# Optimization experiments

Measured on AMD Instinct MI355X. Metric: run time of the kernel, lower is better.

The kernel has to match this reference:

```python
import jax, jax.numpy as jnp
import numpy as np

B, V, H, W = 1, 88, 128, 256
P = 2                  # patch size
D = 128                # hidden_dim = embed_dim // latent_ratio = 1536 // 12
NG = 12                # n_group (== latent_ratio)
NH = 2                 # heads per attention = num_heads // latent_ratio = 24 // 12
E = NG * D             # embed_dim = 1536
HD = D // NH
SCALE = HD ** -0.5

# Static ragged group index sets derived from the variable names (sizes 7,7,7,7,7,9,9,9,9,9,17,6).
# Pressure-level vars are ordered z,q,t,u,v per level; levels [50..400]=7 levels, [50..600]=9 levels.
_off = {'z': 0, 'q': 1, 't': 2, 'u': 3, 'v': 4}
GROUPS = []
for name in ['u1', 'v1', 't1', 'q1', 'z1', 'u2', 'v2', 't2', 'q2', 'z2', 'surf', 'const']:
    if name[-1] in '12':
        nl = 7 if name[-1] == '1' else 9
        GROUPS.append(np.array([5 * li + _off[name[0]] for li in range(nl)]))
    elif name == 'surf':
        GROUPS.append(np.arange(65, 82))   # 17 surface vars
    else:
        GROUPS.append(np.arange(82, 88))   # 6 constant vars


def setup_inputs() -> dict:
    key = jax.random.key(0)
    ks = jax.random.split(key, 16)
    return {
        "x": jax.random.normal(ks[0], (B, V, H, W), jnp.float32),
        # per-variable conv patch-embed weights, flattened to (V, P*P, D)
        "conv_w": jax.random.normal(ks[1], (V, P * P, D), jnp.float32) * 0.05,
        "conv_b": jax.random.normal(ks[2], (V, D), jnp.float32) * 0.02,
        "channel_embed": jax.random.normal(ks[3], (1, V, D), jnp.float32) * 0.02,
        "channel_query": jax.random.uniform(ks[4], (1, NG, D), jnp.float32) * 0.2,
        # 12 distinct MultiheadAttention modules: packed in_proj (3D, D) + out_proj
        "grp_in_w": jax.random.normal(ks[5], (NG, 3 * D, D), jnp.float32) * 0.05,
        "grp_in_b": jax.random.normal(ks[6], (NG, 3 * D), jnp.float32) * 0.02,
        "grp_out_w": jax.random.normal(ks[7], (NG, D, D), jnp.float32) * 0.05,
        "grp_out_b": jax.random.normal(ks[8], (NG, D), jnp.float32) * 0.02,
        "ens_query": jax.random.uniform(ks[9], (1, NG, D), jnp.float32) * 0.2,
        "ens_in_w": jax.random.normal(ks[10], (3 * D, D), jnp.float32) * 0.05,
        "ens_in_b": jax.random.normal(ks[11], (3 * D,), jnp.float32) * 0.02,
        "ens_out_w": jax.random.normal(ks[12], (D, D), jnp.float32) * 0.05,
        "ens_out_b": jax.random.normal(ks[13], (D,), jnp.float32) * 0.02,
        "ln_gamma": jnp.ones((E,), jnp.float32),
        "ln_beta": jnp.zeros((E,), jnp.float32),
    }


def reference(x, conv_w, conv_b, channel_embed, channel_query,
              grp_in_w, grp_in_b, grp_out_w, grp_out_b,
              ens_query, ens_in_w, ens_in_b, ens_out_w, ens_out_b,
              ln_gamma, ln_beta):
    b, v, h, w = x.shape
    hp, wp = h // P, w // P
    L = hp * wp
    # non-overlapping stride-P conv with 1 input channel == patchify + per-variable matmul
    patches = x.reshape(b, v, hp, P, wp, P).transpose(0, 1, 2, 4, 3, 5).reshape(b, v, L, P * P)
    xe = jnp.einsum('bvlp,vpd->bvld', patches, conv_w) + conv_b[None, :, None, :]
    xe = xe + channel_embed[:, :, None, :]                 # (B, V, L, D)
    xn = xe.transpose(0, 2, 1, 3).reshape(b * L, v, D)     # (N, V, D), N = B*L

    outs = []
    for i, ids in enumerate(GROUPS):                       # 12 fixed, structurally distinct groups
        kv = xn[:, ids, :]                                 # (N, g, D), ragged g
        Wq, Wk, Wv = grp_in_w[i, :D], grp_in_w[i, D:2 * D], grp_in_w[i, 2 * D:]
        bq, bk, bv = grp_in_b[i, :D], grp_in_b[i, D:2 * D], grp_in_b[i, 2 * D:]
        q = (channel_query[0, i] @ Wq.T + bq).reshape(NH, HD)
        k = (kv @ Wk.T + bk).reshape(-1, len(ids), NH, HD)
        vv = (kv @ Wv.T + bv).reshape(-1, len(ids), NH, HD)
        a = jax.nn.softmax(jnp.einsum('hd,nghd->nhg', q, k) * SCALE, axis=-1)
        o = jnp.einsum('nhg,nghd->nhd', a, vv).reshape(-1, D)
        outs.append(o @ grp_out_w[i].T + grp_out_b[i])
    out = jnp.stack(outs, axis=1)                          # (N, 12, D)

    Wq, Wk, Wv = ens_in_w[:D], ens_in_w[D:2 * D], ens_in_w[2 * D:]
    bq, bk, bv = ens_in_b[:D], ens_in_b[D:2 * D], ens_in_b[2 * D:]
    q = (ens_query[0] @ Wq.T + bq).reshape(NG, NH, HD)     # 12 ensemble query tokens
    k = (out @ Wk.T + bk).reshape(-1, NG, NH, HD)
    vv = (out @ Wv.T + bv).reshape(-1, NG, NH, HD)
    a = jax.nn.softmax(jnp.einsum('thd,nshd->nhts', q, k) * SCALE, axis=-1)
    r = jnp.einsum('nhts,nshd->nthd', a, vv).reshape(-1, NG, D)
    r = (r @ ens_out_w.T + ens_out_b).reshape(b, L, E)     # (B, L, embed_dim)

    mu = r.mean(axis=-1, keepdims=True)
    var = r.var(axis=-1, keepdims=True)
    return (r - mu) * jax.lax.rsqrt(var + 1e-5) * ln_gamma + ln_beta
```

## Files before the change

kernel.cpp:

```cpp
#include <hip/hip_runtime.h>


typedef __attribute__((ext_vector_type(8))) short short8;
typedef __attribute__((ext_vector_type(4))) float f32x4;

__constant__ int GOFF[13] = {0,7,14,21,28,35,44,53,62,71,80,97,103};
__constant__ int K5A[12]  = {35,35,35,35,35,45,45,45,45,45,85,30};
__constant__ int SLOTS3[12] = {3,3,3,3,3,3,3,3,3,3,6,2};
__constant__ int FOFFA[12] = {0,3,6,9,12,15,18,21,24,27,30,36};
__constant__ int GSLOT[103] = {
  3,8,13,18,23,28,33,
  4,9,14,19,24,29,34,
  2,7,12,17,22,27,32,
  1,6,11,16,21,26,31,
  0,5,10,15,20,25,30,
  3,8,13,18,23,28,33,38,43,
  4,9,14,19,24,29,34,39,44,
  2,7,12,17,22,27,32,37,42,
  1,6,11,16,21,26,31,36,41,
  0,5,10,15,20,25,30,35,40,
  45,46,47,48,49,50,51,52,53,54,55,56,57,58,59,60,61,
  62,63,64,65,66,67};
__constant__ int GIDX[103] = {
  0,0,0,0,0,0,0, 1,1,1,1,1,1,1, 2,2,2,2,2,2,2, 3,3,3,3,3,3,3, 4,4,4,4,4,4,4,
  5,5,5,5,5,5,5,5,5, 6,6,6,6,6,6,6,6,6, 7,7,7,7,7,7,7,7,7, 8,8,8,8,8,8,8,8,8,
  9,9,9,9,9,9,9,9,9,
  10,10,10,10,10,10,10,10,10,10,10,10,10,10,10,10,10,
  11,11,11,11,11,11};
__constant__ int TGI[38] = {0,0,0,1,1,1,2,2,2,3,3,3,4,4,4,5,5,5,6,6,6,7,7,7,
                            8,8,8,9,9,9,10,10,10,10,10,10,11,11};
__constant__ int TNT[38] = {0,1,2,0,1,2,0,1,2,0,1,2,0,1,2,0,1,2,0,1,2,0,1,2,
                            0,1,2,0,1,2,0,1,2,3,4,5,0,1};

constexpr int cSLOTS[12] = {3,3,3,3,3,3,3,3,3,3,6,2};
constexpr int cFOFFA[12] = {0,3,6,9,12,15,18,21,24,27,30,36};

#define QK_GRP 0
#define QK_ENS 3072
#define QB_GRP 6144
#define QB_ENS 6176
#define CGRP   6208
#define CENS   7744
#define CWQ_BYTE   43776
#define MPL_BYTE   50432
#define CW2_BYTE   836864
#define MEB_BYTE   1623296
#define QKEB_BYTE  1688832
#define FWS_BYTE   1697024

__device__ __forceinline__ float bf2f(unsigned short s) {
  return __uint_as_float(((unsigned)s) << 16);
}
__device__ __forceinline__ unsigned short f2bf(float f) {
  unsigned u = __float_as_uint(f);
  u += 0x7fffu + ((u >> 16) & 1u);
  return (unsigned short)(u >> 16);
}

__global__ void hwe_p1(const float* __restrict__ giw, const float* __restrict__ gib,
                       const float* __restrict__ gow, const float* __restrict__ gob,
                       const float* __restrict__ cq,  const float* __restrict__ eq,
                       const float* __restrict__ eiw, const float* __restrict__ eib,
                       const float* __restrict__ eow, const float* __restrict__ eob,
                       const float* __restrict__ cw,  const float* __restrict__ cb,
                       const float* __restrict__ ce,
                       float* __restrict__ wsf, unsigned short* __restrict__ MA,
                       unsigned short* __restrict__ CW2,
                       unsigned short* __restrict__ MeB, unsigned short* __restrict__ Fws) {
  int blk = blockIdx.x, tid = threadIdx.x;
  int wave = tid >> 6, lane = tid & 63;
  if (blk < 48) {
    __shared__ float qf[64];
    bool ens = blk >= 24;
    int bi = ens ? blk - 24 : blk;
    int i = bi >> 1, h = bi & 1;
    const float* W  = ens ? eiw : giw + i*49152;
    const float* bv = ens ? eib : gib + i*384;
    const float* qv = ens ? eq + i*128 : cq + i*128;
    for (int it = 0; it < 16; ++it) {
      int dp = it*4 + wave;
      const float* wrow = W + (h*64 + dp)*128;
      float acc = wrow[lane]*qv[lane] + wrow[lane+64]*qv[lane+64];
#pragma unroll
      for (int off = 32; off > 0; off >>= 1) acc += __shfl_down(acc, off);
      if (lane == 0) qf[dp] = acc + bv[h*64 + dp];
    }
    __syncthreads();
    if (tid < 128) {
      int e = tid;
      const float* Wk = W + (128 + h*64)*128 + e;
      float a0=0.f,a1=0.f,a2=0.f,a3=0.f;
      for (int dp = 0; dp < 64; dp += 4) {
        a0 += qf[dp+0] * Wk[(dp+0)*128];
        a1 += qf[dp+1] * Wk[(dp+1)*128];
        a2 += qf[dp+2] * Wk[(dp+2)*128];
        a3 += qf[dp+3] * Wk[(dp+3)*128];
      }
      wsf[(ens ? QK_ENS : QK_GRP) + bi*128 + e] = (a0+a1)+(a2+a3);
    }
    if (wave == 3) {
      float acc = qf[lane] * bv[128 + h*64 + lane];
#pragma unroll
      for (int off = 32; off > 0; off >>= 1) acc += __shfl_down(acc, off);
      if (lane == 0) wsf[(ens ? QB_ENS : QB_GRP) + bi] = acc;
    }
  } else if (blk < 1584) {
    int b2 = blk - 48;
    int gi = b2 >> 7, r = b2 & 127;
    int ep = tid, h = ep >> 7, e = ep & 127;
    const float* wo = gow + gi*16384 + r*128 + h*64;
    const float* wv = giw + gi*49152 + (256 + h*64)*128 + e;
    float a0=0.f,a1=0.f,a2=0.f,a3=0.f;
    for (int hd = 0; hd < 64; hd += 4) {
      a0 += wo[hd+0] * wv[(hd+0)*128];
      a1 += wo[hd+1] * wv[(hd+1)*128];
      a2 += wo[hd+2] * wv[(hd+2)*128];
      a3 += wo[hd+3] * wv[(hd+3)*128];
    }
    float acc = (a0+a1)+(a2+a3);
    int mt = r >> 4, lr = r & 15, kt = e >> 5, q = (e >> 3) & 3, j = e & 7;
    MA[(((gi*2 + h)*8 + mt)*4 + kt)*512 + (q*16 + lr)*8 + j] = f2bf(acc);
  } else if (blk < 1712) {
    int f2 = (blk - 1584)*256 + tid;
    int r = f2 >> 8, ep = f2 & 255;
    int h = ep >> 7, e = ep & 127;
    const float* wo = eow + r*128 + h*64;
    const float* wv = eiw + (256 + h*64)*128 + e;
    float a0=0.f,a1=0.f,a2=0.f,a3=0.f;
    for (int hd = 0; hd < 64; hd += 4) {
      a0 += wo[hd+0] * wv[(hd+0)*128];
      a1 += wo[hd+1] * wv[(hd+1)*128];
      a2 += wo[hd+2] * wv[(hd+2)*128];
      a3 += wo[hd+3] * wv[(hd+3)*128];
    }
    float acc = (a0+a1)+(a2+a3);
    int mt = r >> 4, lr = r & 15, kt = ep >> 5, q = (ep >> 3) & 3, j = ep & 7;
    MeB[((mt*8 + kt)*64 + (q*16 + lr))*8 + j] = f2bf(acc);
  } else if (blk < 2096) {
    int id = (blk - 1712)*4 + wave;
    int i = id >> 7, d = id & 127;
    const float* wrow = gow + i*16384 + d*128;
    const float* bvv = gib + i*384 + 256;
    float acc = wrow[lane]*bvv[lane] + wrow[lane+64]*bvv[lane+64];
#pragma unroll
    for (int off = 32; off > 0; off >>= 1) acc += __shfl_down(acc, off);
    if (lane == 0) wsf[CGRP + id] = acc + gob[i*128 + d];
  } else if (blk < 2128) {
    int d = (blk - 2096)*4 + wave;
    const float* wrow = eow + d*128;
    const float* bvv = eib + 256;
    float acc = wrow[lane]*bvv[lane] + wrow[lane+64]*bvv[lane+64];
#pragma unroll
    for (int off = 32; off > 0; off >>= 1) acc += __shfl_down(acc, off);
    if (lane == 0) wsf[CENS + d] = acc + eob[d];
  } else if (blk < 2166) {
    int tile = blk - 2128;
    int gi = TGI[tile], nt = TNT[tile];
    int kt = tid >> 6;
    int l15b = tid & 15, quadb = (tid >> 4) & 3;
    int k = nt*16 + l15b;
    int e = kt*32 + quadb*8;
    unsigned short vv[8];
    if (k < K5A[gi]) {
      int q = (k*205) >> 10;
      int pp = k - q*5;
      int s = GSLOT[GOFF[gi] + q];
      int v = (s < 45) ? s : s + 20;
      if (pp < 4) {
        const float* src = cw + (v*4 + pp)*128 + e;
#pragma unroll
        for (int j = 0; j < 8; ++j) vv[j] = f2bf(src[j]);
      } else {
        const float* b1 = cb + v*128 + e;
        const float* c1 = ce + v*128 + e;
#pragma unroll
        for (int j = 0; j < 8; ++j) vv[j] = f2bf(b1[j] + c1[j]);
      }
    } else {
#pragma unroll
      for (int j = 0; j < 8; ++j) vv[j] = 0;
    }
    unsigned short* dst = CW2 + (tile*4 + kt)*512 + (tid & 63)*8;
#pragma unroll
    for (int j = 0; j < 8; ++j) dst[j] = vv[j];
  } else {
    int idx = (blk - 2166)*256 + tid;
    if (idx < 19456) ((uint4*)Fws)[idx] = (uint4){0,0,0,0};
  }
}

__global__ void hwe_p2(const float* __restrict__ cw, const float* __restrict__ cb,
                       const float* __restrict__ ce,
                       const unsigned short* __restrict__ MA,
                       const unsigned short* __restrict__ CW2,
                       const float* __restrict__ wsf,
                       unsigned short* __restrict__ Fws,
                       unsigned short* __restrict__ qkeB, float* __restrict__ cwq) {
  int blk = blockIdx.x, tid = threadIdx.x;
  int wave = tid >> 6, lane = tid & 63;
  int quad = lane >> 4, l15 = lane & 15;
  if (blk < 192) {
    int gi = blk >> 4, h = (blk >> 3) & 1, mt = blk & 7;
    int K5 = K5A[gi], S = SLOTS3[gi];
    const unsigned short* MAp = MA + (((gi*2 + h)*8 + mt)*4)*512 + lane*8;
    short8 a[4];
#pragma unroll
    for (int kt = 0; kt < 4; ++kt)
      a[kt] = *(const short8*)(MAp + kt*512);
    for (int nt = wave; nt < S; nt += 4) {
      const unsigned short* Bp = CW2 + (FOFFA[gi] + nt)*2048 + lane*8;
      f32x4 acc = {0.f,0.f,0.f,0.f};
#pragma unroll
      for (int kt = 0; kt < 4; ++kt) {
        short8 b = *(const short8*)(Bp + kt*512);
        acc = __builtin_amdgcn_mfma_f32_16x16x32_bf16(a[kt], b, acc, 0, 0, 0);
      }
      int k = nt*16 + l15;
      if (k < K5) {
        int kpp = h*K5 + k;
        int base = (FOFFA[gi]*8 + mt*S + (kpp >> 5))*512
                 + ((kpp >> 3) & 3)*128 + (kpp & 7);
#pragma unroll
        for (int reg = 0; reg < 4; ++reg) {
          int rr = quad*4 + reg;
          Fws[base + rr*8] = f2bf(acc[reg]);
        }
      }
    }
  } else if (blk < 208) {
    int f4 = (blk - 192)*256 + tid;
    int ln = (f4 >> 3) & 63, j = f4 & 7;
    int th = ((f4 >> 11) & 1)*16 + (ln & 15);
    int kt = (f4 >> 9) & 3;
    float val = (th < 24) ? wsf[QK_ENS + th*128 + kt*32 + (ln >> 4)*8 + j] : 0.f;
    qkeB[f4] = f2bf(val);
  } else {
    int wid = (blk - 208)*4 + wave;
    if (wid < 206) {
      int gg = wid >> 1, h = wid & 1;
      int gi = GIDX[gg];
      int s = GSLOT[gg];
      int v = (s < 45) ? s : s + 20;
      const float* qk = wsf + QK_GRP + (gi*2 + h)*128;
      float q0 = qk[lane], q1 = qk[lane + 64];
      float a[5];
#pragma unroll
      for (int pp = 0; pp < 4; ++pp)
        a[pp] = cw[(v*4 + pp)*128 + lane]*q0 + cw[(v*4 + pp)*128 + lane + 64]*q1;
      a[4] = (cb[v*128 + lane] + ce[v*128 + lane])*q0 +
             (cb[v*128 + lane + 64] + ce[v*128 + lane + 64])*q1;
#pragma unroll
      for (int off = 32; off > 0; off >>= 1)
#pragma unroll
        for (int kk = 0; kk < 5; ++kk) a[kk] += __shfl_down(a[kk], off);
      if (lane == 0) {
        float* o = cwq + (gg*2 + h)*8;
        o[0] = a[0]*0.125f; o[1] = a[1]*0.125f; o[2] = a[2]*0.125f; o[3] = a[3]*0.125f;
        o[4] = (a[4] + wsf[QB_GRP + gi*2 + h]) * 0.125f;
      }
    }
  }
}

__global__ __launch_bounds__(256, 3) void hwe_main(
    const float* __restrict__ x,
    const float* __restrict__ lgam, const float* __restrict__ lbet,
    const float* __restrict__ wsf,  const float* __restrict__ cwq,
    const unsigned short* __restrict__ Fws, const unsigned short* __restrict__ MeB,
    const unsigned short* __restrict__ qkeB,
    float* __restrict__ out) {
  __shared__ __align__(16) unsigned char smem[53632];
  unsigned short* xpB   = (unsigned short*)(smem);
  unsigned short* scb   = (unsigned short*)(smem + 4352);
  unsigned short* wpAll = (unsigned short*)(smem + 7680);
  unsigned short* Gl    = (unsigned short*)(smem);
  unsigned short* apB   = (unsigned short*)(smem + 20480);
  unsigned short* sce2  = (unsigned short*)(smem);
  unsigned short* outg2 = (unsigned short*)(smem + 28672);
  float*          stats = (float*)(smem + 53504);

  const int tid  = threadIdx.x;
  const int wave = tid >> 6;
  const int lane = tid & 63;
  const int quad = lane >> 4;
  const int l15  = lane & 15;

  const int hi   = blockIdx.x >> 4;
  const int wib  = (blockIdx.x & 15) << 3;
  const int nbase = hi*128 + wib;

  for (int idx = tid; idx < 1088; idx += 256) {
    int c2 = idx & 7, r = (idx >> 3) & 1, s = idx >> 4;
    int v = (s < 45) ? s : s + 20;
    const float2 xv = *(const float2*)(x + (v*128 + 2*hi + r)*256 + 2*wib + c2*2);
    unsigned pk = (unsigned)f2bf(xv.x) | ((unsigned)f2bf(xv.y) << 16);
    *(unsigned*)(xpB + (c2*68 + s)*4 + r*2) = pk;
  }
  if (tid < 64) ((unsigned*)outg2)[96*64 + tid] = 0u;
  __syncthreads();

  for (int idx = tid; idx < 1648; idx += 256) {
    int h = idx & 1, p = (idx >> 1) & 7, gg = idx >> 4;
    int s = GSLOT[gg];
    const float* c = cwq + (gg*2 + h)*8;
    const unsigned short* xr = xpB + (p*68 + s)*4;
    float acc = c[4] + bf2f(xr[0])*c[0] + bf2f(xr[1])*c[1]
                     + bf2f(xr[2])*c[2] + bf2f(xr[3])*c[3];
    scb[(p*2 + h)*104 + gg] = f2bf(acc);
  }
  __syncthreads();

  if (tid < 192) {
    int gi = tid % 12, h = (tid / 12) & 1, p = tid / 24;
    int go = GOFF[gi], G = GOFF[gi+1] - go;
    unsigned short* row = scb + (p*2 + h)*104 + go;
    float ev[17];
    float m = -1e30f;
#pragma unroll
    for (int g = 0; g < 17; ++g) {
      ev[g] = (g < G) ? bf2f(row[g]) : -1e30f;
      m = fmaxf(m, ev[g]);
    }
    float ssum = 0.f;
#pragma unroll
    for (int g = 0; g < 17; ++g) {
      float e = __expf(ev[g] - m);
      ev[g] = e;
      if (g < G) ssum += e;
    }
    float inv = 1.f / ssum;
#pragma unroll
    for (int g = 0; g < 17; ++g)
      if (g < G) row[g] = f2bf(ev[g] * inv);
  }
  __syncthreads();

#pragma unroll
  for (int hb = 0; hb < 2; ++hb) {
    const int nsl = hb ? 20 : 18;
    const int sbase = hb ? 18 : 0;

    short8 fA[6], fB[6];
    float4 cgA, cgB;
    auto fws_issue = [&](int I, short8 (&buf)[6], float4& cg) {
      int gi = hb*6 + (I >> 1);
      int S  = cSLOTS[gi];
      int mt = (I & 1)*4 + wave;
      const unsigned short* fp = Fws + (cFOFFA[gi]*8 + mt*S)*512 + lane*8;
#pragma unroll
      for (int kt = 0; kt < 6; ++kt)
        if (kt < S) buf[kt] = *(const short8*)(fp + kt*512);
      cg = *(const float4*)(wsf + CGRP + gi*128 + mt*16 + quad*4);
    };
    auto fws_compute = [&](int I, short8 (&buf)[6], const float4& cg) {
      int gi = hb*6 + (I >> 1);
      int S  = cSLOTS[gi];
      int mt = (I & 1)*4 + wave;
      int lbase = cFOFFA[gi] - sbase;
      f32x4 acc = {0.f,0.f,0.f,0.f};
#pragma unroll
      for (int kt = 0; kt < 6; ++kt)
        if (kt < S) {
          short8 b = *(const short8*)(wpAll + (lbase + kt)*512 + lane*8);
          acc = __builtin_amdgcn_mfma_f32_16x16x32_bf16(buf[kt], b, acc, 0, 0, 0);
        }
      if (l15 < 8) {
        int p = l15;
        int rb = mt*16 + quad*4;
        unsigned short t0 = f2bf(acc[0] + cg.x);
        unsigned short t1 = f2bf(acc[1] + cg.y);
        unsigned short t2 = f2bf(acc[2] + cg.z);
        unsigned short t3 = f2bf(acc[3] + cg.w);
        uint2 w;
        w.x = (unsigned)t0 | ((unsigned)t1 << 16);
        w.y = (unsigned)t2 | ((unsigned)t3 << 16);
        int row = gi*8 + p;
        int ch = (rb >> 3) ^ ((gi ^ p) & 7);
        *(uint2*)(outg2 + row*128 + ch*8 + (rb & 7)) = w;
      }
    };

    fws_issue(0, fA, cgA);

    {
      const int nposs = nsl * 512;
      for (int pos = tid*4; pos < nposs; pos += 1024) {
        int pf = (pos >> 3) & 15;
        uint2 w2 = {0u, 0u};
        if (pf < 8) {
          int ls = pos >> 9;
          int qd = (pos >> 7) & 3;
          int j0 = pos & 7;
          int p  = pf;
          int gil, K5, fo, goffB, c0, stp;
          if (hb == 0) {
            gil = (ls>=3)+(ls>=6)+(ls>=9)+(ls>=12)+(ls>=15);
            K5 = (gil < 5) ? 35 : 45;
            fo = gil*3;
            goffB = gil*7;
            c0 = (gil==0)?3:(gil==1)?4:(gil==2)?2:(gil==3)?1:(gil==4)?0:3;
            stp = 5;
          } else {
            gil = (ls>=3)+(ls>=6)+(ls>=9)+(ls>=12)+(ls>=18);
            K5 = (gil < 4) ? 45 : (gil == 4) ? 85 : 30;
            fo = (gil < 5) ? gil*3 : 18;
            goffB = (gil < 5) ? (44 + gil*9) : 97;
            c0 = (gil==0)?4:(gil==1)?2:(gil==2)?1:(gil==3)?0:(gil==4)?45:62;
            stp = (gil < 4) ? 5 : 1;
          }
          int kbase = (ls - fo)*32 + qd*8 + j0;
          unsigned short vv[4];
#pragma unroll
          for (int jj = 0; jj < 4; ++jj) {
            int kpp = kbase + jj;
            int h = (kpp >= K5) ? 1 : 0;
            int k = kpp - (h ? K5 : 0);
            int q = (k*205) >> 10;
            int pp = k - q*5;
            int gg = goffB + q;
            int s = c0 + q*stp;
            float a  = bf2f(scb[(p*2 + h)*104 + gg]);
            float xv = bf2f(xpB[(p*68 + s)*4 + pp]);
            float val = (pp < 4) ? a * xv : a;
            if (kpp >= 2*K5) val = 0.f;
            vv[jj] = f2bf(val);
          }
          w2.x = (unsigned)vv[0] | ((unsigned)vv[1] << 16);
          w2.y = (unsigned)vv[2] | ((unsigned)vv[3] << 16);
        }
        *(uint2*)(wpAll + pos) = w2;
      }
    }
    __syncthreads();

#pragma unroll
    for (int ii = 0; ii < 6; ++ii) {
      fws_issue(ii*2 + 1, fB, cgB);
      fws_compute(ii*2, fA, cgA);
      if (ii < 5) fws_issue(ii*2 + 2, fA, cgA);
      fws_compute(ii*2 + 1, fB, cgB);
    }
    __syncthreads();
  }

#pragma unroll
  for (int ti = 0; ti < 3; ++ti) {
    int T = wave*3 + ti;
    int mtp = T >> 1, ntp = T & 1;
    int rowA = mtp*16 + l15;
    int sx = ((rowA >> 3) ^ rowA) & 7;
    f32x4 acc = {0.f,0.f,0.f,0.f};
#pragma unroll
    for (int kt = 0; kt < 4; ++kt) {
      short8 a = *(const short8*)(outg2 + rowA*128 + (((kt*4 + quad) ^ sx) << 3));
      short8 b = *(const short8*)(qkeB + ((ntp*4 + kt)*64 + lane)*8);
      acc = __builtin_amdgcn_mfma_f32_16x16x32_bf16(a, b, acc, 0, 0, 0);
    }
    int th = ntp*16 + l15;
    if (th < 24) {
      float qb = wsf[QB_ENS + th];
#pragma unroll
      for (int reg = 0; reg < 4; ++reg) {
        int rowE = mtp*16 + quad*4 + reg;
        sce2[((rowE & 7)*24 + th)*16 + (rowE >> 3)] = f2bf((acc[reg] + qb) * 0.125f);
      }
    }
  }
  __syncthreads();

  if (tid < 192) {
    unsigned short* row = sce2 + tid*16;
    float ev[12];
    float m = -1e30f;
#pragma unroll
    for (int s = 0; s < 12; ++s) { ev[s] = bf2f(row[s]); m = fmaxf(m, ev[s]); }
    float ssum = 0.f;
#pragma unroll
    for (int s = 0; s < 12; ++s) { float e = __expf(ev[s] - m); ev[s] = e; ssum += e; }
    float inv = 1.f / ssum;
#pragma unroll
    for (int s = 0; s < 12; ++s) row[s] = f2bf(ev[s] * inv);
  }
  __syncthreads();

  for (int idx = tid; idx < 4096; idx += 256) {
    int p = idx >> 9, r9 = idx & 511;
    int ln = r9 >> 3, j = r9 & 7;
    int t = ln & 15, qd = ln >> 4;
    int kpp = qd*8 + j;
    int h = kpp >> 4, s = kpp & 15;
    unsigned short v = 0;
    if (s < 12 && t < 12) v = sce2[(p*24 + t*2 + h)*16 + s];
    apB[p*512 + ln*8 + j] = v;
  }
  float cens0[4], cens1[4];
  {
    float4 c0 = *(const float4*)(wsf + CENS + (wave*2 + 0)*16 + quad*4);
    float4 c1 = *(const float4*)(wsf + CENS + (wave*2 + 1)*16 + quad*4);
    cens0[0]=c0.x; cens0[1]=c0.y; cens0[2]=c0.z; cens0[3]=c0.w;
    cens1[0]=c1.x; cens1[1]=c1.y; cens1[2]=c1.z; cens1[3]=c1.w;
  }
  short8 meAr[16];
#pragma unroll
  for (int mi = 0; mi < 2; ++mi)
#pragma unroll
    for (int h = 0; h < 2; ++h)
#pragma unroll
      for (int kt = 0; kt < 4; ++kt)
        meAr[(mi*2 + h)*4 + kt] =
          *(const short8*)(MeB + (((wave*2 + mi)*8 + h*4 + kt)*64 + lane)*8);
  __syncthreads();

  for (int pp2 = 0; pp2 < 4; ++pp2) {
    f32x4 g[2][2][2];
#pragma unroll
    for (int lp = 0; lp < 2; ++lp)
#pragma unroll
      for (int mi = 0; mi < 2; ++mi)
#pragma unroll
        for (int h = 0; h < 2; ++h) g[lp][mi][h] = (f32x4){0.f,0.f,0.f,0.f};
#pragma unroll
    for (int lp = 0; lp < 2; ++lp) {
      int p = pp2*2 + lp;
      int brow = (l15 < 12) ? (l15*8 + p) : 96;
      int sx = ((brow >> 3) ^ brow) & 7;
#pragma unroll
      for (int h = 0; h < 2; ++h) {
#pragma unroll
        for (int kt = 0; kt < 4; ++kt) {
          short8 b = *(const short8*)(outg2 + brow*128 + (((kt*4 + quad) ^ sx) << 3));
          g[lp][0][h] = __builtin_amdgcn_mfma_f32_16x16x32_bf16(
              meAr[(0*2 + h)*4 + kt], b, g[lp][0][h], 0, 0, 0);
          g[lp][1][h] = __builtin_amdgcn_mfma_f32_16x16x32_bf16(
              meAr[(1*2 + h)*4 + kt], b, g[lp][1][h], 0, 0, 0);
        }
      }
    }
#pragma unroll
    for (int lp = 0; lp < 2; ++lp)
#pragma unroll
      for (int mi = 0; mi < 2; ++mi)
#pragma unroll
        for (int h = 0; h < 2; ++h)
#pragma unroll
          for (int reg = 0; reg < 4; ++reg) {
            int r = (wave*2 + mi)*16 + quad*4 + reg;
            Gl[lp*5120 + r*40 + h*16 + l15] = f2bf(g[lp][mi][h][reg]);
          }

    f32x4 rr[2][2];
    float s1[2] = {0.f, 0.f}, s2[2] = {0.f, 0.f};
#pragma unroll
    for (int lp = 0; lp < 2; ++lp) {
      int p = pp2*2 + lp;
      short8 bfrag = *(const short8*)(apB + p*512 + lane*8);
#pragma unroll
      for (int mi = 0; mi < 2; ++mi) {
        int mt2 = wave*2 + mi;
        short8 afrag = *(const short8*)(Gl + lp*5120 + (mt2*16 + l15)*40 + quad*8);
        f32x4 acc = {0.f,0.f,0.f,0.f};
        acc = __builtin_amdgcn_mfma_f32_16x16x32_bf16(afrag, bfrag, acc, 0, 0, 0);
#pragma unroll
        for (int reg = 0; reg < 4; ++reg)
          acc[reg] += (mi ? cens1[reg] : cens0[reg]);
        rr[lp][mi] = acc;
        if (l15 < 12) {
#pragma unroll
          for (int reg = 0; reg < 4; ++reg) {
            float v = acc[reg];
            s1[lp] += v; s2[lp] += v*v;
          }
        }
      }
    }
#pragma unroll
    for (int off = 32; off > 0; off >>= 1) {
#pragma unroll
      for (int lp = 0; lp < 2; ++lp) {
        s1[lp] += __shfl_xor(s1[lp], off);
        s2[lp] += __shfl_xor(s2[lp], off);
      }
    }
    int sb = (pp2 & 1) << 4;
    if (lane == 0) {
#pragma unroll
      for (int lp = 0; lp < 2; ++lp) {
        stats[sb + lp*4 + wave] = s1[lp];
        stats[sb + 8 + lp*4 + wave] = s2[lp];
      }
    }
    __syncthreads();
#pragma unroll
    for (int lp = 0; lp < 2; ++lp) {
      float t1 = stats[sb+lp*4+0] + stats[sb+lp*4+1] + stats[sb+lp*4+2] + stats[sb+lp*4+3];
      float t2 = stats[sb+8+lp*4+0] + stats[sb+8+lp*4+1] + stats[sb+8+lp*4+2] + stats[sb+8+lp*4+3];
      float mean = t1 * (1.f/1536.f);
      float var  = t2 * (1.f/1536.f) - mean*mean;
      float rstd = rsqrtf(var + 1e-5f);
      if (l15 < 12) {
        long nrow = (long)(nbase + pp2*2 + lp) * 1536;
#pragma unroll
        for (int mi = 0; mi < 2; ++mi) {
          int rb = (wave*2 + mi)*16 + quad*4;
          int j = l15*128 + rb;
          float4 gm = *(const float4*)(lgam + j);
          float4 bt = *(const float4*)(lbet + j);
          float4 o;
          o.x = (rr[lp][mi][0] - mean)*rstd*gm.x + bt.x;
          o.y = (rr[lp][mi][1] - mean)*rstd*gm.y + bt.y;
          o.z = (rr[lp][mi][2] - mean)*rstd*gm.z + bt.z;
          o.w = (rr[lp][mi][3] - mean)*rstd*gm.w + bt.w;
          *(float4*)(out + nrow + j) = o;
        }
      }
    }
  }
}

extern "C" void kernel_launch(void* const* d_in, const int* in_sizes, int n_in,
                              void* d_out, int out_size, void* d_ws, size_t ws_size,
                              hipStream_t stream) {
  const float* x   = (const float*)d_in[0];
  const float* cw  = (const float*)d_in[1];
  const float* cb  = (const float*)d_in[2];
  const float* ce  = (const float*)d_in[3];
  const float* cq  = (const float*)d_in[4];
  const float* giw = (const float*)d_in[5];
  const float* gib = (const float*)d_in[6];
  const float* gow = (const float*)d_in[7];
  const float* gob = (const float*)d_in[8];
  const float* eq  = (const float*)d_in[9];
  const float* eiw = (const float*)d_in[10];
  const float* eib = (const float*)d_in[11];
  const float* eow = (const float*)d_in[12];
  const float* eob = (const float*)d_in[13];
  const float* lg  = (const float*)d_in[14];
  const float* lb  = (const float*)d_in[15];

  float* wsf = (float*)d_ws;
  float* cwq = (float*)((char*)d_ws + CWQ_BYTE);
  unsigned short* MA   = (unsigned short*)((char*)d_ws + MPL_BYTE);
  unsigned short* CW2  = (unsigned short*)((char*)d_ws + CW2_BYTE);
  unsigned short* MeB  = (unsigned short*)((char*)d_ws + MEB_BYTE);
  unsigned short* qkeB = (unsigned short*)((char*)d_ws + QKEB_BYTE);
  unsigned short* Fws  = (unsigned short*)((char*)d_ws + FWS_BYTE);

  hwe_p1<<<2242, 256, 0, stream>>>(giw, gib, gow, gob, cq, eq, eiw, eib, eow, eob,
                                   cw, cb, ce, wsf, MA, CW2, MeB, Fws);
  hwe_p2<<<260, 256, 0, stream>>>(cw, cb, ce, MA, CW2, wsf, Fws, qkeB, cwq);
  hwe_main<<<1024, 256, 0, stream>>>(x, lg, lb, wsf, cwq, Fws, MeB, qkeB,
                                     (float*)d_out);
}
```

Baseline: 177.6 us.

## Shrink LDS footprint to raise occupancy from 3 to 4 blocks per CU

Reduces the kernel's shared memory from about 53.6KB to 40.6KB and raises launch bounds to 4 blocks per CU. To fit, it stages the grouped-attention weighted inputs in six two-group phases instead of two six-group halves, and packs the softmax score buffer more tightly. It also drops the apB staging buffer by building MFMA B fragments directly from the score buffer, and reuses a single Gl tile per position. The cost is more barriers and phases, extra per-lane masking work, and added register pressure under the tighter launch bound.

```diff
diff --git a/kernel.cpp b/kernel.cpp
--- a/kernel.cpp
+++ b/kernel.cpp
@@ -34,6 +34,10 @@
 
 constexpr int cSLOTS[12] = {3,3,3,3,3,3,3,3,3,3,6,2};
 constexpr int cFOFFA[12] = {0,3,6,9,12,15,18,21,24,27,30,36};
+constexpr int cK5[12]    = {35,35,35,35,35,45,45,45,45,45,85,30};
+constexpr int cGOFFC[12] = {0,7,14,21,28,35,44,53,62,71,80,97};
+constexpr int cC0[12]    = {3,4,2,1,0,3,4,2,1,0,45,62};
+constexpr int cSTP[12]   = {5,5,5,5,5,5,5,5,5,5,1,1};
 
 #define QK_GRP 0
 #define QK_ENS 3072
@@ -262,22 +266,21 @@
   }
 }
 
-__global__ __launch_bounds__(256, 3) void hwe_main(
+__global__ __launch_bounds__(256, 4) void hwe_main(
     const float* __restrict__ x,
     const float* __restrict__ lgam, const float* __restrict__ lbet,
     const float* __restrict__ wsf,  const float* __restrict__ cwq,
     const unsigned short* __restrict__ Fws, const unsigned short* __restrict__ MeB,
     const unsigned short* __restrict__ qkeB,
     float* __restrict__ out) {
-  __shared__ __align__(16) unsigned char smem[53632];
+  __shared__ __align__(16) unsigned char smem[40576];
   unsigned short* xpB   = (unsigned short*)(smem);
   unsigned short* scb   = (unsigned short*)(smem + 4352);
   unsigned short* wpAll = (unsigned short*)(smem + 7680);
   unsigned short* Gl    = (unsigned short*)(smem);
-  unsigned short* apB   = (unsigned short*)(smem + 20480);
-  unsigned short* sce2  = (unsigned short*)(smem);
-  unsigned short* outg2 = (unsigned short*)(smem + 28672);
-  float*          stats = (float*)(smem + 53504);
+  unsigned short* sce2  = (unsigned short*)(smem + 10240);
+  unsigned short* outg2 = (unsigned short*)(smem + 15872);
+  float*          stats = (float*)(smem + 40448);
 
   const int tid  = threadIdx.x;
   const int wave = tid >> 6;
@@ -296,7 +299,6 @@
     unsigned pk = (unsigned)f2bf(xv.x) | ((unsigned)f2bf(xv.y) << 16);
     *(unsigned*)(xpB + (c2*68 + s)*4 + r*2) = pk;
   }
-  if (tid < 64) ((unsigned*)outg2)[96*64 + tid] = 0u;
   __syncthreads();
 
   for (int idx = tid; idx < 1648; idx += 256) {
@@ -335,28 +337,22 @@
   }
   __syncthreads();
 
-#pragma unroll
-  for (int hb = 0; hb < 2; ++hb) {
-    const int nsl = hb ? 20 : 18;
-    const int sbase = hb ? 18 : 0;
-
+  {
     short8 fA[6], fB[6];
     float4 cgA, cgB;
-    auto fws_issue = [&](int I, short8 (&buf)[6], float4& cg) {
-      int gi = hb*6 + (I >> 1);
-      int S  = cSLOTS[gi];
-      int mt = (I & 1)*4 + wave;
+    auto fws_issue = [&](int gi, int mh, short8 (&buf)[6], float4& cg) {
+      int S = cSLOTS[gi];
+      int mt = mh*4 + wave;
       const unsigned short* fp = Fws + (cFOFFA[gi]*8 + mt*S)*512 + lane*8;
 #pragma unroll
       for (int kt = 0; kt < 6; ++kt)
         if (kt < S) buf[kt] = *(const short8*)(fp + kt*512);
       cg = *(const float4*)(wsf + CGRP + gi*128 + mt*16 + quad*4);
     };
-    auto fws_compute = [&](int I, short8 (&buf)[6], const float4& cg) {
-      int gi = hb*6 + (I >> 1);
-      int S  = cSLOTS[gi];
-      int mt = (I & 1)*4 + wave;
-      int lbase = cFOFFA[gi] - sbase;
+    auto fws_compute = [&](int gi, int mh, int lbase, short8 (&buf)[6],
+                           const float4& cg) {
+      int S = cSLOTS[gi];
+      int mt = mh*4 + wave;
       f32x4 acc = {0.f,0.f,0.f,0.f};
 #pragma unroll
       for (int kt = 0; kt < 6; ++kt)
@@ -380,68 +376,83 @@
       }
     };
 
-    fws_issue(0, fA, cgA);
-
-    {
-      const int nposs = nsl * 512;
-      for (int pos = tid*4; pos < nposs; pos += 1024) {
-        int pf = (pos >> 3) & 15;
-        uint2 w2 = {0u, 0u};
-        if (pf < 8) {
-          int ls = pos >> 9;
-          int qd = (pos >> 7) & 3;
-          int j0 = pos & 7;
-          int p  = pf;
-          int gil, K5, fo, goffB, c0, stp;
-          if (hb == 0) {
-            gil = (ls>=3)+(ls>=6)+(ls>=9)+(ls>=12)+(ls>=15);
-            K5 = (gil < 5) ? 35 : 45;
-            fo = gil*3;
-            goffB = gil*7;
-            c0 = (gil==0)?3:(gil==1)?4:(gil==2)?2:(gil==3)?1:(gil==4)?0:3;
-            stp = 5;
-          } else {
-            gil = (ls>=3)+(ls>=6)+(ls>=9)+(ls>=12)+(ls>=18);
-            K5 = (gil < 4) ? 45 : (gil == 4) ? 85 : 30;
-            fo = (gil < 5) ? gil*3 : 18;
-            goffB = (gil < 5) ? (44 + gil*9) : 97;
-            c0 = (gil==0)?4:(gil==1)?2:(gil==2)?1:(gil==3)?0:(gil==4)?45:62;
-            stp = (gil < 4) ? 5 : 1;
+    fws_issue(0, 0, fA, cgA);
+
+#pragma unroll
+    for (int ph = 0; ph < 6; ++ph) {
+      const int g0 = 2*ph;
+      const int S0 = cSLOTS[g0];
+      const int nsl = S0 + cSLOTS[g0+1];
+
+      {
+        const int nposs = nsl * 512;
+        for (int pos = tid*4; pos < nposs; pos += 1024) {
+          int pf = (pos >> 3) & 15;
+          uint2 w2 = {0u, 0u};
+          if (pf < 8) {
+            int ls = pos >> 9;
+            int qd = (pos >> 7) & 3;
+            int j0 = pos & 7;
+            int p  = pf;
+            bool gsel = (ls >= S0);
+            int lsl   = gsel ? ls - S0 : ls;
+            int K5    = gsel ? cK5[g0+1]    : cK5[g0];
+            int goffB = gsel ? cGOFFC[g0+1] : cGOFFC[g0];
+            int c0    = gsel ? cC0[g0+1]    : cC0[g0];
+            int stp   = gsel ? cSTP[g0+1]   : cSTP[g0];
+            int kbase = lsl*32 + qd*8 + j0;
+            unsigned short vv[4];
+#pragma unroll
+            for (int jj = 0; jj < 4; ++jj) {
+              int kpp = kbase + jj;
+              int h = (kpp >= K5) ? 1 : 0;
+              int k = kpp - (h ? K5 : 0);
+              int q = (k*205) >> 10;
+              int pp = k - q*5;
+              int gg = goffB + q;
+              int s = c0 + q*stp;
+              float a  = bf2f(scb[(p*2 + h)*104 + gg]);
+              float xv = bf2f(xpB[(p*68 + s)*4 + pp]);
+              float val = (pp < 4) ? a * xv : a;
+              if (kpp >= 2*K5) val = 0.f;
+              vv[jj] = f2bf(val);
+            }
+            w2.x = (unsigned)vv[0] | ((unsigned)vv[1] << 16);
+            w2.y = (unsigned)vv[2] | ((unsigned)vv[3] << 16);
           }
-          int kbase = (ls - fo)*32 + qd*8 + j0;
-          unsigned short vv[4];
-#pragma unroll
-          for (int jj = 0; jj < 4; ++jj) {
-            int kpp = kbase + jj;
-            int h = (kpp >= K5) ? 1 : 0;
-            int k = kpp - (h ? K5 : 0);
-            int q = (k*205) >> 10;
-            int pp = k - q*5;
-            int gg = goffB + q;
-            int s = c0 + q*stp;
-            float a  = bf2f(scb[(p*2 + h)*104 + gg]);
-            float xv = bf2f(xpB[(p*68 + s)*4 + pp]);
-            float val = (pp < 4) ? a * xv : a;
-            if (kpp >= 2*K5) val = 0.f;
-            vv[jj] = f2bf(val);
-          }
-          w2.x = (unsigned)vv[0] | ((unsigned)vv[1] << 16);
-          w2.y = (unsigned)vv[2] | ((unsigned)vv[3] << 16);
+          *(uint2*)(wpAll + pos) = w2;
         }
-        *(uint2*)(wpAll + pos) = w2;
-      }
-    }
-    __syncthreads();
-
-#pragma unroll
-    for (int ii = 0; ii < 6; ++ii) {
-      fws_issue(ii*2 + 1, fB, cgB);
-      fws_compute(ii*2, fA, cgA);
-      if (ii < 5) fws_issue(ii*2 + 2, fA, cgA);
-      fws_compute(ii*2 + 1, fB, cgB);
-    }
-    __syncthreads();
-  }
+      }
+      __syncthreads();
+
+      fws_issue(g0+0, 1, fB, cgB);
+      fws_compute(g0+0, 0, 0,  fA, cgA);
+      fws_issue(g0+1, 0, fA, cgA);
+      fws_compute(g0+0, 1, 0,  fB, cgB);
+      fws_issue(g0+1, 1, fB, cgB);
+      fws_compute(g0+1, 0, S0, fA, cgA);
+      if (ph < 5) fws_issue(g0+2, 0, fA, cgA);
+      fws_compute(g0+1, 1, S0, fB, cgB);
+      __syncthreads();
+    }
+  }
+
+  float cens0[4], cens1[4];
+  {
+    float4 c0 = *(const float4*)(wsf + CENS + (wave*2 + 0)*16 + quad*4);
+    float4 c1 = *(const float4*)(wsf + CENS + (wave*2 + 1)*16 + quad*4);
+    cens0[0]=c0.x; cens0[1]=c0.y; cens0[2]=c0.z; cens0[3]=c0.w;
+    cens1[0]=c1.x; cens1[1]=c1.y; cens1[2]=c1.z; cens1[3]=c1.w;
+  }
+  short8 meAr[16];
+#pragma unroll
+  for (int mi = 0; mi < 2; ++mi)
+#pragma unroll
+    for (int h = 0; h < 2; ++h)
+#pragma unroll
+      for (int kt = 0; kt < 4; ++kt)
+        meAr[(mi*2 + h)*4 + kt] =
+          *(const short8*)(MeB + (((wave*2 + mi)*8 + h*4 + kt)*64 + lane)*8);
 
 #pragma unroll
   for (int ti = 0; ti < 3; ++ti) {
@@ -462,14 +473,14 @@
 #pragma unroll
       for (int reg = 0; reg < 4; ++reg) {
         int rowE = mtp*16 + quad*4 + reg;
-        sce2[((rowE & 7)*24 + th)*16 + (rowE >> 3)] = f2bf((acc[reg] + qb) * 0.125f);
+        sce2[((rowE & 7)*24 + th)*12 + (rowE >> 3)] = f2bf((acc[reg] + qb) * 0.125f);
       }
     }
   }
   __syncthreads();
 
   if (tid < 192) {
-    unsigned short* row = sce2 + tid*16;
+    unsigned short* row = sce2 + tid*12;
     float ev[12];
     float m = -1e30f;
 #pragma unroll
@@ -483,34 +494,6 @@
   }
   __syncthreads();
 
-  for (int idx = tid; idx < 4096; idx += 256) {
-    int p = idx >> 9, r9 = idx & 511;
-    int ln = r9 >> 3, j = r9 & 7;
-    int t = ln & 15, qd = ln >> 4;
-    int kpp = qd*8 + j;
-    int h = kpp >> 4, s = kpp & 15;
-    unsigned short v = 0;
-    if (s < 12 && t < 12) v = sce2[(p*24 + t*2 + h)*16 + s];
-    apB[p*512 + ln*8 + j] = v;
-  }
-  float cens0[4], cens1[4];
-  {
-    float4 c0 = *(const float4*)(wsf + CENS + (wave*2 + 0)*16 + quad*4);
-    float4 c1 = *(const float4*)(wsf + CENS + (wave*2 + 1)*16 + quad*4);
-    cens0[0]=c0.x; cens0[1]=c0.y; cens0[2]=c0.z; cens0[3]=c0.w;
-    cens1[0]=c1.x; cens1[1]=c1.y; cens1[2]=c1.z; cens1[3]=c1.w;
-  }
-  short8 meAr[16];
-#pragma unroll
-  for (int mi = 0; mi < 2; ++mi)
-#pragma unroll
-    for (int h = 0; h < 2; ++h)
-#pragma unroll
-      for (int kt = 0; kt < 4; ++kt)
-        meAr[(mi*2 + h)*4 + kt] =
-          *(const short8*)(MeB + (((wave*2 + mi)*8 + h*4 + kt)*64 + lane)*8);
-  __syncthreads();
-
   for (int pp2 = 0; pp2 < 4; ++pp2) {
     f32x4 g[2][2][2];
 #pragma unroll
@@ -522,13 +505,14 @@
 #pragma unroll
     for (int lp = 0; lp < 2; ++lp) {
       int p = pp2*2 + lp;
-      int brow = (l15 < 12) ? (l15*8 + p) : 96;
+      int brow = (l15 < 12) ? (l15*8 + p) : 0;
       int sx = ((brow >> 3) ^ brow) & 7;
 #pragma unroll
       for (int h = 0; h < 2; ++h) {
 #pragma unroll
         for (int kt = 0; kt < 4; ++kt) {
           short8 b = *(const short8*)(outg2 + brow*128 + (((kt*4 + quad) ^ sx) << 3));
+          if (l15 >= 12) b = (short8){0,0,0,0,0,0,0,0};
           g[lp][0][h] = __builtin_amdgcn_mfma_f32_16x16x32_bf16(
               meAr[(0*2 + h)*4 + kt], b, g[lp][0][h], 0, 0, 0);
           g[lp][1][h] = __builtin_amdgcn_mfma_f32_16x16x32_bf16(
@@ -536,8 +520,12 @@
         }
       }
     }
-#pragma unroll
-    for (int lp = 0; lp < 2; ++lp)
+
+    f32x4 rr[2][2];
+    float s1[2] = {0.f, 0.f}, s2[2] = {0.f, 0.f};
+#pragma unroll
+    for (int lp = 0; lp < 2; ++lp) {
+      int p = pp2*2 + lp;
 #pragma unroll
       for (int mi = 0; mi < 2; ++mi)
 #pragma unroll
@@ -545,21 +533,24 @@
 #pragma unroll
           for (int reg = 0; reg < 4; ++reg) {
             int r = (wave*2 + mi)*16 + quad*4 + reg;
-            Gl[lp*5120 + r*40 + h*16 + l15] = f2bf(g[lp][mi][h][reg]);
+            Gl[r*40 + h*16 + l15] = f2bf(g[lp][mi][h][reg]);
           }
-
-    f32x4 rr[2][2];
-    float s1[2] = {0.f, 0.f}, s2[2] = {0.f, 0.f};
-#pragma unroll
-    for (int lp = 0; lp < 2; ++lp) {
-      int p = pp2*2 + lp;
-      short8 bfrag = *(const short8*)(apB + p*512 + lane*8);
+      short8 af0 = *(const short8*)(Gl + ((wave*2 + 0)*16 + l15)*40 + quad*8);
+      short8 af1 = *(const short8*)(Gl + ((wave*2 + 1)*16 + l15)*40 + quad*8);
+      union { short8 s8; uint4 u4; } bu;
+      {
+        const unsigned short* sp = sce2 + (p*24 + l15*2 + (quad >> 1))*12 + (quad & 1)*8;
+        uint2 lo = *(const uint2*)(sp);
+        uint2 hi2 = *(const uint2*)(sp + 4);
+        if (quad & 1) { hi2.x = 0u; hi2.y = 0u; }
+        if (l15 >= 12) { lo.x = 0u; lo.y = 0u; hi2.x = 0u; hi2.y = 0u; }
+        bu.u4.x = lo.x; bu.u4.y = lo.y; bu.u4.z = hi2.x; bu.u4.w = hi2.y;
+      }
 #pragma unroll
       for (int mi = 0; mi < 2; ++mi) {
-        int mt2 = wave*2 + mi;
-        short8 afrag = *(const short8*)(Gl + lp*5120 + (mt2*16 + l15)*40 + quad*8);
         f32x4 acc = {0.f,0.f,0.f,0.f};
-        acc = __builtin_amdgcn_mfma_f32_16x16x32_bf16(afrag, bfrag, acc, 0, 0, 0);
+        acc = __builtin_amdgcn_mfma_f32_16x16x32_bf16(mi ? af1 : af0, bu.s8,
+                                                      acc, 0, 0, 0);
 #pragma unroll
         for (int reg = 0; reg < 4; ++reg)
           acc[reg] += (mi ? cens1[reg] : cens0[reg]);
```

Result: slower. 182.1 us (+2.5%).
